# Kernel tuning notes

Hardware: AMD Instinct MI355X
Metric: run time of the kernel (lower is better)

Reference implementation:

```python
import jax, jax.numpy as jnp
import numpy as np

# irreps config (l<=1 only)
N, E = 20000, 400000
NS, NV = 64, 32          # node: 64x0e + 32x1o  (dim 64 + 96 = 160)
ES, EV = 8, 8            # edge: 8x0e + 8x1o    (dim 8 + 24 = 32)
HS, HV = 96, 32          # hidden: 96x0e + 32x1o (last HV scalars are gates)
GS = HS - HV             # post-gate scalar channels
INV_SQRT3 = float(1.0 / np.sqrt(3.0))  # w3j(1,1,0) normalization


def _tp_gate(xs, xv, ys, yv, Wss, Wvv, Wsv, Wvs):
    """FullyConnectedTensorProduct (paths 0x0->0, 1.1->0, 0x1->1, 1x0->1)
    with fan-in path normalization, followed by a gated nonlinearity:
    silu on scalars, sigmoid-gated vectors.
    xs:[*,u] xv:[*,u',3] ys:[*,v] yv:[*,v',3] -> (gs:[*,GS], gv:[*,HV,3])"""
    n_s = 1.0 / np.sqrt(Wss.shape[0] * Wss.shape[1] + Wvv.shape[0] * Wvv.shape[1])
    n_v = 1.0 / np.sqrt(Wsv.shape[0] * Wsv.shape[1] + Wvs.shape[0] * Wvs.shape[1])
    hs = (jnp.einsum('eu,ev,uvw->ew', xs, ys, Wss)
          + INV_SQRT3 * jnp.einsum('euk,evk,uvw->ew', xv, yv, Wvv)) * n_s
    hv = (jnp.einsum('eu,evk,uvw->ewk', xs, yv, Wsv)
          + jnp.einsum('euk,ev,uvw->ewk', xv, ys, Wvs)) * n_v
    gs = jax.nn.silu(hs[:, :GS])
    gates = jax.nn.sigmoid(hs[:, GS:])          # [*, HV]
    gv = hv * gates[:, :, None]
    return gs, gv


def _irrep_linear(s, v, Ws, Wv):
    """e3nn-style Linear: independent multiplicity mixing per irrep, 1/sqrt(fan_in)."""
    return (s @ Ws) / np.sqrt(Ws.shape[0]), jnp.einsum('nuk,uw->nwk', v, Wv) / np.sqrt(Wv.shape[0])


def setup_inputs() -> dict:
    key = jax.random.key(0)
    ks = jax.random.split(key, 16)
    inp = {
        'node_features': jax.random.normal(ks[0], (N, NS + 3 * NV), jnp.float32),
        'edge_attr_tensor': jax.random.normal(ks[1], (E, ES + 3 * EV), jnp.float32),
        'node_attr_scalar_raw': jax.random.normal(ks[2], (N, 1), jnp.float32),
        'edge_index': jax.random.randint(ks[3], (2, E), 0, N),
        # message TP weights: node (x) edge -> hidden
        'W_m_ss': jax.random.normal(ks[4], (NS, ES, HS), jnp.float32),
        'W_m_vv': jax.random.normal(ks[5], (NV, EV, HS), jnp.float32),
        'W_m_sv': jax.random.normal(ks[6], (NS, EV, HV), jnp.float32),
        'W_m_vs': jax.random.normal(ks[7], (NV, ES, HV), jnp.float32),
        # linear_messages_out: gate-out (GSx0e+HVx1o) -> hidden
        'Wl_ms': jax.random.normal(ks[8], (GS, HS), jnp.float32),
        'Wl_mv': jax.random.normal(ks[9], (HV, HV), jnp.float32),
        # update TP weights: node (x) hidden -> hidden
        'W_u_ss': jax.random.normal(ks[10], (NS, HS, HS), jnp.float32),
        'W_u_vv': jax.random.normal(ks[11], (NV, HV, HS), jnp.float32),
        'W_u_sv': jax.random.normal(ks[12], (NS, HV, HV), jnp.float32),
        'W_u_vs': jax.random.normal(ks[13], (NV, HS, HV), jnp.float32),
        # linear_update_out: gate-out -> node irreps
        'Wl_us': jax.random.normal(ks[14], (GS, NS), jnp.float32),
        'Wl_uv': jax.random.normal(ks[15], (HV, NV), jnp.float32),
    }
    return inp


def reference(node_features, edge_attr_tensor, node_attr_scalar_raw, edge_index,
              W_m_ss, W_m_vv, W_m_sv, W_m_vs, Wl_ms, Wl_mv,
              W_u_ss, W_u_vv, W_u_sv, W_u_vs, Wl_us, Wl_uv):
    n = node_features.shape[0]
    row, col = edge_index[0], edge_index[1]
    xs = node_features[:, :NS]                              # [N,NS]
    xv = node_features[:, NS:].reshape(n, NV, 3)            # [N,NV,3]
    es = edge_attr_tensor[:, :ES]                           # [E,ES]
    ev = edge_attr_tensor[:, ES:].reshape(-1, EV, 3)        # [E,EV,3]
    # gather source nodes, TP with edge attrs, gate
    ms, mv = _tp_gate(xs[col], xv[col], es, ev, W_m_ss, W_m_vv, W_m_sv, W_m_vs)
    ms, mv = _irrep_linear(ms, mv, Wl_ms, Wl_mv)            # -> hidden irreps
    # scatter-sum into destination nodes
    ags = jax.ops.segment_sum(ms, row, num_segments=n)      # [N,HS]
    agv = jax.ops.segment_sum(mv.reshape(-1, HV * 3), row, num_segments=n).reshape(n, HV, 3)
    # update TP: node (x) aggregated, gate, project back to node irreps
    us, uv = _tp_gate(xs, xv, ags, agv, W_u_ss, W_u_vv, W_u_sv, W_u_vs)
    us, uv = _irrep_linear(us, uv, Wl_us, Wl_uv)
    upd = jnp.concatenate([us, uv.reshape(n, NV * 3)], axis=-1)
    return node_features + upd
```

## Files before the change

### kernel.cpp

```cpp
#include <hip/hip_runtime.h>

#define NN 20000
#define NE 400000

typedef __attribute__((ext_vector_type(4))) float f32x4;
typedef _Float16 h2 __attribute__((ext_vector_type(2)));
typedef _Float16 h8 __attribute__((ext_vector_type(8)));

union H8 { h8 v; h2 p[4]; };

__device__ __forceinline__ float sigf(float x) { return 1.0f / (1.0f + __expf(-x)); }

__device__ __forceinline__ h8 rank1(_Float16 x, const h2 e[4]) {
    h2 xb = {x, x}; H8 f;
    #pragma unroll
    for (int j = 0; j < 4; ++j) f.p[j] = xb * e[j];
    return f.v;
}
__device__ __forceinline__ h8 rank3(_Float16 x0, _Float16 x1, _Float16 x2,
                                    const h2 e0[4], const h2 e1[4], const h2 e2[4]) {
    h2 x0b = {x0, x0}, x1b = {x1, x1}, x2b = {x2, x2}; H8 f;
    #pragma unroll
    for (int j = 0; j < 4; ++j) f.p[j] = x0b * e0[j] + x1b * e1[j] + x2b * e2[j];
    return f.v;
}
#define MFMA(a, b, c) __builtin_amdgcn_mfma_f32_16x16x32_f16(a, b, c, 0, 0, 0)

__global__ void prep_kernel(const float* __restrict__ s1, const float* __restrict__ s2,
                            int K1, int Kt, int Nw, float sc1, float sc2,
                            unsigned short* __restrict__ dst, int total)
{
    int idx = blockIdx.x * 256 + threadIdx.x;
    if (idx >= total) return;
    int w = idx / Kt, K = idx - w * Kt;
    float v = (K < K1) ? s1[(size_t)K * Nw + w] * sc1
                       : s2[(size_t)(K - K1) * Nw + w] * sc2;
    _Float16 h = (_Float16)v;
    dst[idx] = __builtin_bit_cast(unsigned short, h);
}

__global__ void hist_kernel(const int* __restrict__ eidx, int* __restrict__ counts)
{
    int e = blockIdx.x * 256 + threadIdx.x;
    if (e < NE) atomicAdd(&counts[eidx[e]], 1);
}

__global__ __launch_bounds__(1024)
void scan_kernel(int* __restrict__ data)
{
    __shared__ int wsum[16];
    __shared__ int s_carry;
    const int t = threadIdx.x, lane = t & 63, wv = t >> 6;
    if (t == 0) s_carry = 0;
    __syncthreads();
    for (int base = 0; base < NN; base += 1024) {
        int carry = s_carry;
        int idx = base + t;
        int v = (idx < NN) ? data[idx] : 0;
        int s = v;
        #pragma unroll
        for (int d = 1; d < 64; d <<= 1) {
            int x = __shfl_up(s, d, 64);
            if (lane >= d) s += x;
        }
        if (lane == 63) wsum[wv] = s;
        __syncthreads();
        if (t < 16) {
            int ws = wsum[t];
            #pragma unroll
            for (int d = 1; d < 16; d <<= 1) {
                int x = __shfl_up(ws, d, 64);
                if (t >= d) ws += x;
            }
            wsum[t] = ws;
        }
        __syncthreads();
        if (idx < NN) data[idx] = carry + (wv ? wsum[wv - 1] : 0) + s - v;
        if (t == 0) s_carry = carry + wsum[15];
        __syncthreads();
    }
}

__global__ void scatter_kernel(const int* __restrict__ eidx, int* __restrict__ cursor,
                               int* __restrict__ perm)
{
    int e = blockIdx.x * 256 + threadIdx.x;
    if (e < NE) {
        int r = eidx[e];
        int p = atomicAdd(&cursor[r], 1);
        perm[p] = e;
    }
}

template<int MB>
__device__ __forceinline__ void msg_gemmB(
    int ln, int okt,
    const _Float16 (*s_xsh)[68], const _Float16 (*s_xv01)[66], const _Float16 (*s_xv2)[34],
    const _Float16 (*s_esh)[8], const _Float16 (*s_evTh)[3][8],
    const unsigned short* __restrict__ wB, f32x4* acc)
{
    const unsigned short* b0p = wB + (size_t)ln * 768;
    const unsigned short* b1p = wB + (size_t)(16 + ln) * 768;

    h2 vv[6][4];
    #pragma unroll
    for (int m = 0; m < 6; ++m) {
        const int k = (MB + m) >> 2, e = (((MB + m) & 3) << 4) + ln;
        #pragma unroll
        for (int j = 0; j < 4; ++j) vv[m][j] = ((const h2*)s_evTh[e][k])[j];
    }
    #pragma unroll 4
    for (int ks = 0; ks < 16; ++ks) {
        const int ko = ks * 32 + okt * 8, u = ks * 4 + okt;
        h8 b0 = *(const h8*)(b0p + ko), b1 = *(const h8*)(b1p + ko);
        #pragma unroll
        for (int m = 0; m < 6; ++m) {
            const int e = (((MB + m) & 3) << 4) + ln;
            h8 a = rank1(s_xsh[e][u], vv[m]);
            acc[m * 2]     = MFMA(a, b0, acc[m * 2]);
            acc[m * 2 + 1] = MFMA(a, b1, acc[m * 2 + 1]);
        }
    }
    h2 ee[6][4];
    #pragma unroll
    for (int m = 0; m < 6; ++m) {
        const int e = (((MB + m) & 3) << 4) + ln;
        #pragma unroll
        for (int j = 0; j < 4; ++j) ee[m][j] = ((const h2*)s_esh[e])[j];
    }
    #pragma unroll 4
    for (int ks = 0; ks < 8; ++ks) {
        const int ko = 512 + ks * 32 + okt * 8, u = ks * 4 + okt;
        h8 b0 = *(const h8*)(b0p + ko), b1 = *(const h8*)(b1p + ko);
        #pragma unroll
        for (int m = 0; m < 6; ++m) {
            const int k = (MB + m) >> 2, e = (((MB + m) & 3) << 4) + ln;
            _Float16 x = (k < 2) ? s_xv01[e][u * 2 + k] : s_xv2[e][u];
            h8 a = rank1(x, ee[m]);
            acc[m * 2]     = MFMA(a, b0, acc[m * 2]);
            acc[m * 2 + 1] = MFMA(a, b1, acc[m * 2 + 1]);
        }
    }
}

__global__ __launch_bounds__(256, 3)
void msg_kernel(const float* __restrict__ nf, const float* __restrict__ ea,
                const int* __restrict__ eidx, const int* __restrict__ perm,
                const unsigned short* __restrict__ wA,
                const unsigned short* __restrict__ wB,
                float* __restrict__ agg)
{
    const int e0 = blockIdx.x * 64;
    const int t = threadIdx.x;
    const int wid = t >> 6, lane = t & 63, ln = lane & 15, okt = lane >> 4;

    __shared__ __align__(16) char smem[41216];
    _Float16 (*s_xsh)[68]    = (_Float16(*)[68])(smem);
    _Float16 (*s_xv01)[66]   = (_Float16(*)[66])(smem + 8704);
    _Float16 (*s_xv2)[34]    = (_Float16(*)[34])(smem + 17152);
    _Float16 (*s_esh)[8]     = (_Float16(*)[8])(smem + 21504);
    _Float16 (*s_evTh)[3][8] = (_Float16(*)[3][8])(smem + 22528);
    float (*s_msg)[161]      = (float(*)[161])(smem);

    __shared__ float s_gate[64][33];
    __shared__ int s_row[64], s_col[64], s_pe[64];

    if (t < 64) {
        int p = perm[e0 + t];
        s_pe[t] = p;
        s_row[t] = eidx[p];
        s_col[t] = eidx[NE + p];
    }
    __syncthreads();
    for (int i = t; i < 64 * 32; i += 256) {
        int e = i >> 5, c = i & 31;
        float v = ea[(size_t)s_pe[e] * 32 + c];
        if (c < 8) s_esh[e][c] = (_Float16)v;
        else { int d = c - 8; s_evTh[e][d % 3][d / 3] = (_Float16)v; }
    }
    for (int i = t; i < 64 * 40; i += 256) {
        int e = i / 40, q = i - e * 40;
        f32x4 f4 = *((const f32x4*)nf + (size_t)s_col[e] * 40 + q);
        if (q < 16) {
            #pragma unroll
            for (int j = 0; j < 4; ++j) s_xsh[e][q * 4 + j] = (_Float16)f4[j];
        } else {
            #pragma unroll
            for (int j = 0; j < 4; ++j) {
                int d = (q - 16) * 4 + j, u = d / 3, k = d - u * 3;
                if (k < 2) s_xv01[e][u * 2 + k] = (_Float16)f4[j];
                else       s_xv2[e][u] = (_Float16)f4[j];
            }
        }
    }
    __syncthreads();

    f32x4 acc[12] = {};

    if (wid < 2) {
        const unsigned short* wb = wA + (size_t)(wid * 48 + ln) * 768;
        h2 esv[4][4];
        #pragma unroll
        for (int m = 0; m < 4; ++m)
            #pragma unroll
            for (int j = 0; j < 4; ++j) esv[m][j] = ((const h2*)s_esh[m * 16 + ln])[j];
        #pragma unroll 4
        for (int ks = 0; ks < 16; ++ks) {
            const int ko = ks * 32 + okt * 8, u = ks * 4 + okt;
            h8 b0 = *(const h8*)(wb + ko);
            h8 b1 = *(const h8*)(wb + 16 * 768 + ko);
            h8 b2 = *(const h8*)(wb + 32 * 768 + ko);
            #pragma unroll
            for (int m = 0; m < 4; ++m) {
                h8 a = rank1(s_xsh[m * 16 + ln][u], esv[m]);
                acc[m * 3 + 0] = MFMA(a, b0, acc[m * 3 + 0]);
                acc[m * 3 + 1] = MFMA(a, b1, acc[m * 3 + 1]);
                acc[m * 3 + 2] = MFMA(a, b2, acc[m * 3 + 2]);
            }
        }
        h2 ev0[4][4], ev1[4][4], ev2[4][4];
        #pragma unroll
        for (int m = 0; m < 4; ++m)
            #pragma unroll
            for (int j = 0; j < 4; ++j) {
                ev0[m][j] = ((const h2*)s_evTh[m * 16 + ln][0])[j];
                ev1[m][j] = ((const h2*)s_evTh[m * 16 + ln][1])[j];
                ev2[m][j] = ((const h2*)s_evTh[m * 16 + ln][2])[j];
            }
        #pragma unroll 4
        for (int ks = 0; ks < 8; ++ks) {
            const int ko = 512 + ks * 32 + okt * 8, u = ks * 4 + okt;
            h8 b0 = *(const h8*)(wb + ko);
            h8 b1 = *(const h8*)(wb + 16 * 768 + ko);
            h8 b2 = *(const h8*)(wb + 32 * 768 + ko);
            #pragma unroll
            for (int m = 0; m < 4; ++m) {
                h2 x01 = *(const h2*)&s_xv01[m * 16 + ln][u * 2];
                h8 a = rank3(x01[0], x01[1], s_xv2[m * 16 + ln][u], ev0[m], ev1[m], ev2[m]);
                acc[m * 3 + 0] = MFMA(a, b0, acc[m * 3 + 0]);
                acc[m * 3 + 1] = MFMA(a, b1, acc[m * 3 + 1]);
                acc[m * 3 + 2] = MFMA(a, b2, acc[m * 3 + 2]);
            }
        }
    } else if (wid == 2) {
        msg_gemmB<0>(ln, okt, s_xsh, s_xv01, s_xv2, s_esh, s_evTh, wB, acc);
    } else {
        msg_gemmB<6>(ln, okt, s_xsh, s_xv01, s_xv2, s_esh, s_evTh, wB, acc);
    }

    __syncthreads();

    if (wid < 2) {
        #pragma unroll
        for (int m = 0; m < 4; ++m)
            #pragma unroll
            for (int j = 0; j < 3; ++j)
                #pragma unroll
                for (int r = 0; r < 4; ++r) {
                    int e = m * 16 + okt * 4 + r;
                    int w = wid * 48 + j * 16 + ln;
                    float h = acc[m * 3 + j][r];
                    if (w < 64) s_msg[e][w] = h * sigf(h);
                    else        s_gate[e][w - 64] = sigf(h);
                }
    }
    __syncthreads();
    if (wid >= 2) {
        const int mb = (wid - 2) * 6;
        #pragma unroll
        for (int m = 0; m < 6; ++m) {
            int mm = mb + m, k = mm >> 2;
            #pragma unroll
            for (int tt = 0; tt < 2; ++tt)
                #pragma unroll
                for (int r = 0; r < 4; ++r) {
                    int e = ((mm & 3) << 4) + okt * 4 + r;
                    int w2 = tt * 16 + ln;
                    s_msg[e][64 + w2 * 3 + k] = acc[m * 2 + tt][r] * s_gate[e][w2];
                }
        }
    }
    __syncthreads();

    if (t < 160) {
        int cur = s_row[0];
        float a = s_msg[0][t];
        for (int e = 1; e < 64; ++e) {
            int r = s_row[e];
            float v = s_msg[e][t];
            if (r != cur) {
                atomicAdd(agg + (size_t)cur * 160 + t, a);
                cur = r; a = v;
            } else a += v;
        }
        atomicAdd(agg + (size_t)cur * 160 + t, a);
    }
}

__global__ __launch_bounds__(256, 2)
void upd_kernel(const float* __restrict__ nf, const float* __restrict__ agg,
                const unsigned short* __restrict__ wA,
                const unsigned short* __restrict__ wB,
                const float* __restrict__ Wlms, const float* __restrict__ Wlmv,
                const float* __restrict__ Wls, const float* __restrict__ Wlv,
                float* __restrict__ out)
{
    const int n0 = blockIdx.x * 32;
    const int t = threadIdx.x;
    const int wid = t >> 6, lane = t & 63, ln = lane & 15, okt = lane >> 4;

    __shared__ __align__(16) _Float16 s_xsh[32][68];
    __shared__ __align__(16) _Float16 s_xv01[32][66];
    __shared__ __align__(16) _Float16 s_xv2[32][34];
    __shared__ __align__(16) _Float16 s_ash[32][104];
    __shared__ __align__(16) _Float16 s_avTh[32][3][40];
    __shared__ float s_hs2[32][100];
    __shared__ float s_hv2[96][34];
    __shared__ float s_ag[32][160];

    for (int i = t; i < 32 * 160; i += 256)
        ((float*)s_ag)[i] = agg[(size_t)n0 * 160 + i];
    for (int i = t; i < 32 * 40; i += 256) {
        int n = i / 40, q = i - n * 40;
        f32x4 f4 = *((const f32x4*)nf + (size_t)(n0 + n) * 40 + q);
        if (q < 16) {
            #pragma unroll
            for (int j = 0; j < 4; ++j) s_xsh[n][q * 4 + j] = (_Float16)f4[j];
        } else {
            #pragma unroll
            for (int j = 0; j < 4; ++j) {
                int d = (q - 16) * 4 + j, u = d / 3, k = d - u * 3;
                if (k < 2) s_xv01[n][u * 2 + k] = (_Float16)f4[j];
                else       s_xv2[n][u] = (_Float16)f4[j];
            }
        }
    }
    __syncthreads();
    #pragma unroll
    for (int r = 0; r < 12; ++r) {
        int o = t + r * 256;
        int n = o / 96, q = o - n * 96;
        float a = 0.f;
        #pragma unroll
        for (int u = 0; u < 64; ++u) a = fmaf(s_ag[n][u], Wlms[u * 96 + q], a);
        s_ash[n][q] = (_Float16)(a * 0.125f);
    }
    #pragma unroll
    for (int r = 0; r < 12; ++r) {
        int o = t + r * 256;
        int n = o / 96, q = o - n * 96, k = q >> 5, v = q & 31;
        float a = 0.f;
        #pragma unroll
        for (int u = 0; u < 32; ++u) a = fmaf(s_ag[n][64 + u * 3 + k], Wlmv[u * 32 + v], a);
        s_avTh[n][k][v] = (_Float16)(a * 0.17677669529663687f);
    }
    __syncthreads();

    f32x4 acc[6] = {};

    if (wid < 2) {
        const unsigned short* wb = wA + (size_t)(wid * 48 + ln) * 7168;
        #pragma unroll 2
        for (int kb = 0; kb < 64; ++kb) {
            _Float16 x0 = s_xsh[ln][kb];
            _Float16 x1 = s_xsh[16 + ln][kb];
            #pragma unroll
            for (int p = 0; p < 3; ++p) {
                const int ko = kb * 96 + p * 32 + okt * 8;
                const int v0 = p * 32 + okt * 8;
                h8 b0 = *(const h8*)(wb + ko);
                h8 b1 = *(const h8*)(wb + 16 * 7168 + ko);
                h8 b2 = *(const h8*)(wb + 32 * 7168 + ko);
                h8 a0 = rank1(x0, (const h2*)&s_ash[ln][v0]);
                h8 a1 = rank1(x1, (const h2*)&s_ash[16 + ln][v0]);
                acc[0] = MFMA(a0, b0, acc[0]); acc[1] = MFMA(a0, b1, acc[1]); acc[2] = MFMA(a0, b2, acc[2]);
                acc[3] = MFMA(a1, b0, acc[3]); acc[4] = MFMA(a1, b1, acc[4]); acc[5] = MFMA(a1, b2, acc[5]);
            }
        }
        #pragma unroll 4
        for (int ks = 0; ks < 32; ++ks) {
            const int ko = 6144 + ks * 32 + okt * 8;
            const int v0 = okt * 8;
            h8 b0 = *(const h8*)(wb + ko);
            h8 b1 = *(const h8*)(wb + 16 * 7168 + ko);
            h8 b2 = *(const h8*)(wb + 32 * 7168 + ko);
            h2 xa = *(const h2*)&s_xv01[ln][ks * 2];
            h2 xb = *(const h2*)&s_xv01[16 + ln][ks * 2];
            h8 a0 = rank3(xa[0], xa[1], s_xv2[ln][ks],
                          (const h2*)&s_avTh[ln][0][v0], (const h2*)&s_avTh[ln][1][v0],
                          (const h2*)&s_avTh[ln][2][v0]);
            h8 a1 = rank3(xb[0], xb[1], s_xv2[16 + ln][ks],
                          (const h2*)&s_avTh[16 + ln][0][v0], (const h2*)&s_avTh[16 + ln][1][v0],
                          (const h2*)&s_avTh[16 + ln][2][v0]);
            acc[0] = MFMA(a0, b0, acc[0]); acc[1] = MFMA(a0, b1, acc[1]); acc[2] = MFMA(a0, b2, acc[2]);
            acc[3] = MFMA(a1, b0, acc[3]); acc[4] = MFMA(a1, b1, acc[4]); acc[5] = MFMA(a1, b2, acc[5]);
        }
    } else {
        const unsigned short* bp = wB + (size_t)((wid - 2) * 16 + ln) * 5120;
        #pragma unroll 2
        for (int ks = 0; ks < 64; ++ks) {
            const int ko = ks * 32 + okt * 8;
            const int v0 = okt * 8;
            h8 b = *(const h8*)(bp + ko);
            #pragma unroll
            for (int m = 0; m < 6; ++m) {
                const int k = m >> 1, n = ((m & 1) << 4) + ln;
                h8 a = rank1(s_xsh[n][ks], (const h2*)&s_avTh[n][k][v0]);
                acc[m] = MFMA(a, b, acc[m]);
            }
        }
        #pragma unroll 2
        for (int kb = 0; kb < 32; ++kb) {
            _Float16 xa[6];
            #pragma unroll
            for (int m = 0; m < 6; ++m) {
                const int k = m >> 1, n = ((m & 1) << 4) + ln;
                xa[m] = (k < 2) ? s_xv01[n][kb * 2 + k] : s_xv2[n][kb];
            }
            #pragma unroll
            for (int p = 0; p < 3; ++p) {
                const int ko = 2048 + kb * 96 + p * 32 + okt * 8;
                const int v0 = p * 32 + okt * 8;
                h8 b = *(const h8*)(bp + ko);
                #pragma unroll
                for (int m = 0; m < 6; ++m) {
                    const int n = ((m & 1) << 4) + ln;
                    h8 a = rank1(xa[m], (const h2*)&s_ash[n][v0]);
                    acc[m] = MFMA(a, b, acc[m]);
                }
            }
        }
    }

    if (wid < 2) {
        #pragma unroll
        for (int m = 0; m < 2; ++m)
            #pragma unroll
            for (int j = 0; j < 3; ++j)
                #pragma unroll
                for (int r = 0; r < 4; ++r)
                    s_hs2[m * 16 + okt * 4 + r][wid * 48 + j * 16 + ln] = acc[m * 3 + j][r];
    } else {
        #pragma unroll
        for (int m = 0; m < 6; ++m)
            #pragma unroll
            for (int r = 0; r < 4; ++r)
                s_hv2[m * 16 + okt * 4 + r][(wid - 2) * 16 + ln] = acc[m][r];
    }
    __syncthreads();
    for (int i = t; i < 32 * 96; i += 256) {
        int n = i / 96, w = i - n * 96;
        float h = s_hs2[n][w];
        s_hs2[n][w] = (w < 64) ? h * sigf(h) : sigf(h);
    }
    __syncthreads();
    for (int i = t; i < 96 * 32; i += 256) {
        int R = i >> 5, w2 = i & 31, n = R & 31;
        s_hv2[R][w2] *= s_hs2[n][64 + w2];
    }
    __syncthreads();
    for (int i = t; i < 32 * 64; i += 256) {
        int n = i >> 6, w = i & 63;
        float a = 0.f;
        #pragma unroll
        for (int u = 0; u < 64; ++u) a = fmaf(s_hs2[n][u], Wls[u * 64 + w], a);
        size_t o = (size_t)(n0 + n) * 160 + w;
        out[o] = nf[o] + a * 0.125f;
    }
    for (int i = t; i < 32 * 96; i += 256) {
        int n = i / 96, wk = i - n * 96, w = wk / 3, k = wk - w * 3;
        float a = 0.f;
        #pragma unroll
        for (int u = 0; u < 32; ++u) a = fmaf(s_hv2[k * 32 + n][u], Wlv[u * 32 + w], a);
        size_t o = (size_t)(n0 + n) * 160 + 64 + wk;
        out[o] = nf[o] + a * 0.17677669529663687f;
    }
}

extern "C" void kernel_launch(void* const* d_in, const int* in_sizes, int n_in,
                              void* d_out, int out_size, void* d_ws, size_t ws_size,
                              hipStream_t stream) {
    const float* nf   = (const float*)d_in[0];
    const float* ea   = (const float*)d_in[1];
    const int*   eidx = (const int*)d_in[3];
    const float* Wmss = (const float*)d_in[4];
    const float* Wmvv = (const float*)d_in[5];
    const float* Wmsv = (const float*)d_in[6];
    const float* Wmvs = (const float*)d_in[7];
    const float* Wlms = (const float*)d_in[8];
    const float* Wlmv = (const float*)d_in[9];
    const float* Wuss = (const float*)d_in[10];
    const float* Wuvv = (const float*)d_in[11];
    const float* Wusv = (const float*)d_in[12];
    const float* Wuvs = (const float*)d_in[13];
    const float* Wlus = (const float*)d_in[14];
    const float* Wluv = (const float*)d_in[15];
    float* out = (float*)d_out;

    float* agg = (float*)d_ws;
    unsigned short* wAm = (unsigned short*)(agg + (size_t)NN * 160);
    unsigned short* wBm = wAm + 96 * 768;
    unsigned short* wAu = wBm + 32 * 768;
    unsigned short* wBu = wAu + (size_t)96 * 7168;
    int* counts = (int*)(wBu + (size_t)32 * 5120);
    int* perm   = counts + NN;

    const float NSM = 0.03608439182435161f;
    const float NSU = 0.011811365506297619f;
    const float NVU = 0.013975424859373686f;
    const float S3  = 0.57735026918962576f;

    hipMemsetAsync(agg, 0, (size_t)NN * 160 * sizeof(float), stream);
    hipMemsetAsync(counts, 0, (size_t)NN * sizeof(int), stream);

    prep_kernel<<<(96 * 768 + 255) / 256, 256, 0, stream>>>(Wmss, Wmvv, 512, 768, 96, NSM, NSM * S3, wAm, 96 * 768);
    prep_kernel<<<(32 * 768 + 255) / 256, 256, 0, stream>>>(Wmsv, Wmvs, 512, 768, 32, NSM, NSM, wBm, 32 * 768);
    prep_kernel<<<(96 * 7168 + 255) / 256, 256, 0, stream>>>(Wuss, Wuvv, 6144, 7168, 96, NSU, NSU * S3, wAu, 96 * 7168);
    prep_kernel<<<(32 * 5120 + 255) / 256, 256, 0, stream>>>(Wusv, Wuvs, 2048, 5120, 32, NVU, NVU, wBu, 32 * 5120);

    hist_kernel<<<(NE + 255) / 256, 256, 0, stream>>>(eidx, counts);
    scan_kernel<<<1, 1024, 0, stream>>>(counts);
    scatter_kernel<<<(NE + 255) / 256, 256, 0, stream>>>(eidx, counts, perm);

    msg_kernel<<<NE / 64, 256, 0, stream>>>(nf, ea, eidx, perm, wAm, wBm, agg);
    upd_kernel<<<NN / 32, 256, 0, stream>>>(nf, agg, wAu, wBu, Wlms, Wlmv, Wlus, Wluv, out);
}
```

Before: 574.9 us.

## Tile-transpose weight prep, shrink LDS via fp16 staging, raise occupancy bounds

The weight prep kernel now transposes through a shared-memory tile, so both its global reads and writes are coalesced. In msg_kernel, the message and gate staging buffers become fp16 and are aliased into the shared scratch, which shrinks LDS so launch bounds can rise to 4 blocks per CU. upd_kernel stops staging the aggregate in LDS, reading it from global memory inside the linear loops instead. It also stores its hidden activations in fp16 and raises its occupancy bound. The costs are extra fp16 rounding of intermediate messages before the atomic sums and possible register spills under the tighter bounds.

Result: slower. 698.1 us (+21.4%).

```diff
diff --git a/kernel.cpp b/kernel.cpp
--- a/kernel.cpp
+++ b/kernel.cpp
@@ -26,17 +26,30 @@
 }
 #define MFMA(a, b, c) __builtin_amdgcn_mfma_f32_16x16x32_f16(a, b, c, 0, 0, 0)
 
-__global__ void prep_kernel(const float* __restrict__ s1, const float* __restrict__ s2,
-                            int K1, int Kt, int Nw, float sc1, float sc2,
-                            unsigned short* __restrict__ dst, int total)
-{
-    int idx = blockIdx.x * 256 + threadIdx.x;
-    if (idx >= total) return;
-    int w = idx / Kt, K = idx - w * Kt;
-    float v = (K < K1) ? s1[(size_t)K * Nw + w] * sc1
-                       : s2[(size_t)(K - K1) * Nw + w] * sc2;
-    _Float16 h = (_Float16)v;
-    dst[idx] = __builtin_bit_cast(unsigned short, h);
+__global__ __launch_bounds__(256)
+void prep_kernel(const float* __restrict__ s1, const float* __restrict__ s2,
+                 int K1, int Kt, int Nw, float sc1, float sc2,
+                 unsigned short* __restrict__ dst)
+{
+    __shared__ _Float16 tile[32][34];
+    const int tx = threadIdx.x & 31, ty = threadIdx.x >> 5;
+    const int K0 = blockIdx.x * 32, w0 = blockIdx.y * 32;
+    #pragma unroll
+    for (int r = 0; r < 4; ++r) {
+        int K = K0 + ty + r * 8, w = w0 + tx;
+        if (K < Kt && w < Nw) {
+            float v = (K < K1) ? s1[(size_t)K * Nw + w] * sc1
+                               : s2[(size_t)(K - K1) * Nw + w] * sc2;
+            tile[ty + r * 8][tx] = (_Float16)v;
+        }
+    }
+    __syncthreads();
+    #pragma unroll
+    for (int r = 0; r < 4; ++r) {
+        int w = w0 + ty + r * 8, K = K0 + tx;
+        if (w < Nw && K < Kt)
+            dst[(size_t)w * Kt + K] = __builtin_bit_cast(unsigned short, tile[tx][ty + r * 8]);
+    }
 }
 
 __global__ void hist_kernel(const int* __restrict__ eidx, int* __restrict__ counts)
@@ -143,7 +156,7 @@
     }
 }
 
-__global__ __launch_bounds__(256, 3)
+__global__ __launch_bounds__(256, 4)
 void msg_kernel(const float* __restrict__ nf, const float* __restrict__ ea,
                 const int* __restrict__ eidx, const int* __restrict__ perm,
                 const unsigned short* __restrict__ wA,
@@ -154,15 +167,15 @@
     const int t = threadIdx.x;
     const int wid = t >> 6, lane = t & 63, ln = lane & 15, okt = lane >> 4;
 
-    __shared__ __align__(16) char smem[41216];
+    __shared__ __align__(16) char smem[25600];
     _Float16 (*s_xsh)[68]    = (_Float16(*)[68])(smem);
     _Float16 (*s_xv01)[66]   = (_Float16(*)[66])(smem + 8704);
     _Float16 (*s_xv2)[34]    = (_Float16(*)[34])(smem + 17152);
     _Float16 (*s_esh)[8]     = (_Float16(*)[8])(smem + 21504);
     _Float16 (*s_evTh)[3][8] = (_Float16(*)[3][8])(smem + 22528);
-    float (*s_msg)[161]      = (float(*)[161])(smem);
-
-    __shared__ float s_gate[64][33];
+    _Float16 (*s_msg)[162]   = (_Float16(*)[162])(smem);
+    _Float16 (*s_gate)[33]   = (_Float16(*)[33])(smem + 20736);
+
     __shared__ int s_row[64], s_col[64], s_pe[64];
 
     if (t < 64) {
@@ -260,8 +273,8 @@
                     int e = m * 16 + okt * 4 + r;
                     int w = wid * 48 + j * 16 + ln;
                     float h = acc[m * 3 + j][r];
-                    if (w < 64) s_msg[e][w] = h * sigf(h);
-                    else        s_gate[e][w - 64] = sigf(h);
+                    if (w < 64) s_msg[e][w] = (_Float16)(h * sigf(h));
+                    else        s_gate[e][w - 64] = (_Float16)sigf(h);
                 }
     }
     __syncthreads();
@@ -276,7 +289,8 @@
                 for (int r = 0; r < 4; ++r) {
                     int e = ((mm & 3) << 4) + okt * 4 + r;
                     int w2 = tt * 16 + ln;
-                    s_msg[e][64 + w2 * 3 + k] = acc[m * 2 + tt][r] * s_gate[e][w2];
+                    s_msg[e][64 + w2 * 3 + k] =
+                        (_Float16)(acc[m * 2 + tt][r] * (float)s_gate[e][w2]);
                 }
         }
     }
@@ -284,10 +298,10 @@
 
     if (t < 160) {
         int cur = s_row[0];
-        float a = s_msg[0][t];
+        float a = (float)s_msg[0][t];
         for (int e = 1; e < 64; ++e) {
             int r = s_row[e];
-            float v = s_msg[e][t];
+            float v = (float)s_msg[e][t];
             if (r != cur) {
                 atomicAdd(agg + (size_t)cur * 160 + t, a);
                 cur = r; a = v;
@@ -297,7 +311,7 @@
     }
 }
 
-__global__ __launch_bounds__(256, 2)
+__global__ __launch_bounds__(256, 4)
 void upd_kernel(const float* __restrict__ nf, const float* __restrict__ agg,
                 const unsigned short* __restrict__ wA,
                 const unsigned short* __restrict__ wB,
@@ -314,12 +328,9 @@
     __shared__ __align__(16) _Float16 s_xv2[32][34];
     __shared__ __align__(16) _Float16 s_ash[32][104];
     __shared__ __align__(16) _Float16 s_avTh[32][3][40];
-    __shared__ float s_hs2[32][100];
-    __shared__ float s_hv2[96][34];
-    __shared__ float s_ag[32][160];
-
-    for (int i = t; i < 32 * 160; i += 256)
-        ((float*)s_ag)[i] = agg[(size_t)n0 * 160 + i];
+    __shared__ _Float16 s_hs2[32][104];
+    __shared__ _Float16 s_hv2[96][34];
+
     for (int i = t; i < 32 * 40; i += 256) {
         int n = i / 40, q = i - n * 40;
         f32x4 f4 = *((const f32x4*)nf + (size_t)(n0 + n) * 40 + q);
@@ -335,14 +346,14 @@
             }
         }
     }
-    __syncthreads();
+    const float* agr = agg + (size_t)n0 * 160;
     #pragma unroll
     for (int r = 0; r < 12; ++r) {
         int o = t + r * 256;
         int n = o / 96, q = o - n * 96;
         float a = 0.f;
         #pragma unroll
-        for (int u = 0; u < 64; ++u) a = fmaf(s_ag[n][u], Wlms[u * 96 + q], a);
+        for (int u = 0; u < 64; ++u) a = fmaf(agr[n * 160 + u], Wlms[u * 96 + q], a);
         s_ash[n][q] = (_Float16)(a * 0.125f);
     }
     #pragma unroll
@@ -351,7 +362,7 @@
         int n = o / 96, q = o - n * 96, k = q >> 5, v = q & 31;
         float a = 0.f;
         #pragma unroll
-        for (int u = 0; u < 32; ++u) a = fmaf(s_ag[n][64 + u * 3 + k], Wlmv[u * 32 + v], a);
+        for (int u = 0; u < 32; ++u) a = fmaf(agr[n * 160 + 64 + u * 3 + k], Wlmv[u * 32 + v], a);
         s_avTh[n][k][v] = (_Float16)(a * 0.17677669529663687f);
     }
     __syncthreads();
@@ -439,31 +450,31 @@
             for (int j = 0; j < 3; ++j)
                 #pragma unroll
                 for (int r = 0; r < 4; ++r)
-                    s_hs2[m * 16 + okt * 4 + r][wid * 48 + j * 16 + ln] = acc[m * 3 + j][r];
+                    s_hs2[m * 16 + okt * 4 + r][wid * 48 + j * 16 + ln] = (_Float16)acc[m * 3 + j][r];
     } else {
         #pragma unroll
         for (int m = 0; m < 6; ++m)
             #pragma unroll
             for (int r = 0; r < 4; ++r)
-                s_hv2[m * 16 + okt * 4 + r][(wid - 2) * 16 + ln] = acc[m][r];
+                s_hv2[m * 16 + okt * 4 + r][(wid - 2) * 16 + ln] = (_Float16)acc[m][r];
     }
     __syncthreads();
     for (int i = t; i < 32 * 96; i += 256) {
         int n = i / 96, w = i - n * 96;
-        float h = s_hs2[n][w];
-        s_hs2[n][w] = (w < 64) ? h * sigf(h) : sigf(h);
+        float h = (float)s_hs2[n][w];
+        s_hs2[n][w] = (_Float16)((w < 64) ? h * sigf(h) : sigf(h));
     }
     __syncthreads();
     for (int i = t; i < 96 * 32; i += 256) {
         int R = i >> 5, w2 = i & 31, n = R & 31;
-        s_hv2[R][w2] *= s_hs2[n][64 + w2];
+        s_hv2[R][w2] = (_Float16)((float)s_hv2[R][w2] * (float)s_hs2[n][64 + w2]);
     }
     __syncthreads();
     for (int i = t; i < 32 * 64; i += 256) {
         int n = i >> 6, w = i & 63;
         float a = 0.f;
         #pragma unroll
-        for (int u = 0; u < 64; ++u) a = fmaf(s_hs2[n][u], Wls[u * 64 + w], a);
+        for (int u = 0; u < 64; ++u) a = fmaf((float)s_hs2[n][u], Wls[u * 64 + w], a);
         size_t o = (size_t)(n0 + n) * 160 + w;
         out[o] = nf[o] + a * 0.125f;
     }
@@ -471,7 +482,7 @@
         int n = i / 96, wk = i - n * 96, w = wk / 3, k = wk - w * 3;
         float a = 0.f;
         #pragma unroll
-        for (int u = 0; u < 32; ++u) a = fmaf(s_hv2[k * 32 + n][u], Wlv[u * 32 + w], a);
+        for (int u = 0; u < 32; ++u) a = fmaf((float)s_hv2[k * 32 + n][u], Wlv[u * 32 + w], a);
         size_t o = (size_t)(n0 + n) * 160 + 64 + wk;
         out[o] = nf[o] + a * 0.17677669529663687f;
     }
@@ -513,10 +524,10 @@
     hipMemsetAsync(agg, 0, (size_t)NN * 160 * sizeof(float), stream);
     hipMemsetAsync(counts, 0, (size_t)NN * sizeof(int), stream);
 
-    prep_kernel<<<(96 * 768 + 255) / 256, 256, 0, stream>>>(Wmss, Wmvv, 512, 768, 96, NSM, NSM * S3, wAm, 96 * 768);
-    prep_kernel<<<(32 * 768 + 255) / 256, 256, 0, stream>>>(Wmsv, Wmvs, 512, 768, 32, NSM, NSM, wBm, 32 * 768);
-    prep_kernel<<<(96 * 7168 + 255) / 256, 256, 0, stream>>>(Wuss, Wuvv, 6144, 7168, 96, NSU, NSU * S3, wAu, 96 * 7168);
-    prep_kernel<<<(32 * 5120 + 255) / 256, 256, 0, stream>>>(Wusv, Wuvs, 2048, 5120, 32, NVU, NVU, wBu, 32 * 5120);
+    prep_kernel<<<dim3(24, 3), 256, 0, stream>>>(Wmss, Wmvv, 512, 768, 96, NSM, NSM * S3, wAm);
+    prep_kernel<<<dim3(24, 1), 256, 0, stream>>>(Wmsv, Wmvs, 512, 768, 32, NSM, NSM, wBm);
+    prep_kernel<<<dim3(224, 3), 256, 0, stream>>>(Wuss, Wuvv, 6144, 7168, 96, NSU, NSU * S3, wAu);
+    prep_kernel<<<dim3(160, 1), 256, 0, stream>>>(Wusv, Wuvs, 2048, 5120, 32, NVU, NVU, wBu);
 
     hist_kernel<<<(NE + 255) / 256, 256, 0, stream>>>(eidx, counts);
     scan_kernel<<<1, 1024, 0, stream>>>(counts);
```
